# Optimization experiments

Measured on AMD Instinct MI355X. Metric: run time of the kernel, lower is better.

The kernel has to match this reference:

```python
import jax, jax.numpy as jnp
import numpy as np

HIDDEN = 1024
NUM_HEADS = 16
HEAD_DIM = HIDDEN // NUM_HEADS
ROPE_BASE = 10000.0


def _rope_cos_sin(seq_len, dtype):
    # inv_freq over even indices of head_dim
    inv_freq = 1.0 / (ROPE_BASE ** (jnp.arange(0, HEAD_DIM, 2, dtype=jnp.float32) / HEAD_DIM))
    t = jnp.arange(seq_len, dtype=jnp.float32)
    freqs = t[:, None] * inv_freq[None, :]            # (S, head_dim/2)
    emb = jnp.concatenate([freqs, freqs], axis=-1)    # (S, head_dim)
    cos = jnp.cos(emb)[None, None, :, :].astype(dtype)
    sin = jnp.sin(emb)[None, None, :, :].astype(dtype)
    return cos, sin


def _rotate_interleaved(x):
    # stack((-x[...,1::2], x[...,::2]), -1).flatten(-2) — interleaved pair rotation
    x1 = x[..., ::2]
    x2 = x[..., 1::2]
    return jnp.stack((-x2, x1), axis=-1).reshape(x.shape)


def _apply_rope(x, cos, sin):
    return x * cos + _rotate_interleaved(x) * sin


def setup_inputs() -> dict:
    key = jax.random.key(0)
    k0, k1, k2, k3, k4 = jax.random.split(key, 5)
    B, S = 2, 2048
    scale = 1.0 / np.sqrt(HIDDEN)
    return {
        "hidden_states": jax.random.normal(k0, (B, S, HIDDEN), dtype=jnp.float32),
        "Wq": jax.random.normal(k1, (HIDDEN, HIDDEN), dtype=jnp.float32) * scale,
        "Wk": jax.random.normal(k2, (HIDDEN, HIDDEN), dtype=jnp.float32) * scale,
        "Wv": jax.random.normal(k3, (HIDDEN, HIDDEN), dtype=jnp.float32) * scale,
        "Wo": jax.random.normal(k4, (HIDDEN, HIDDEN), dtype=jnp.float32) * scale,
    }


def reference(hidden_states, Wq, Wk, Wv, Wo):
    B, S, _ = hidden_states.shape
    # torch Linear: y = x @ W.T  (W is (out, in))
    def proj(x, W):
        y = jnp.einsum('bsd,ed->bse', x, W)
        return y.reshape(B, S, NUM_HEADS, HEAD_DIM).transpose(0, 2, 1, 3)  # (B,H,S,Dh)

    q = proj(hidden_states, Wq)
    k = proj(hidden_states, Wk)
    v = proj(hidden_states, Wv)

    cos, sin = _rope_cos_sin(S, hidden_states.dtype)
    q = _apply_rope(q, cos, sin)
    k = _apply_rope(k, cos, sin)

    scores = jnp.einsum('bhqd,bhkd->bhqk', q, k) / jnp.sqrt(jnp.asarray(HEAD_DIM, hidden_states.dtype))
    attn = jax.nn.softmax(scores, axis=-1)
    out = jnp.einsum('bhqk,bhkd->bhqd', attn, v)
    out = out.transpose(0, 2, 1, 3).reshape(B, S, HIDDEN)
    return jnp.einsum('bsd,ed->bse', out, Wo)
```

## Files before the change

kernel.cpp:

```cpp
#include <hip/hip_runtime.h>

typedef __attribute__((ext_vector_type(4)))  float  f32x4;
typedef __attribute__((ext_vector_type(16))) float  f32x16;
typedef __attribute__((ext_vector_type(8)))  short  s16x8;

__device__ __forceinline__ unsigned short f2bf(float f) {
    union { float f; unsigned u; } v; v.f = f;
    unsigned u = v.u + 0x7fffu + ((v.u >> 16) & 1u);
    return (unsigned short)(u >> 16);
}

__device__ __forceinline__ unsigned cvtpk(float lo, float hi_) {
    unsigned r;
    asm("v_cvt_pk_bf16_f32 %0, %1, %2" : "=v"(r) : "v"(lo), "v"(hi_));
    return r;
}

__device__ __forceinline__ void gl_lds16(const unsigned short* g, unsigned short* l) {
    __builtin_amdgcn_global_load_lds(
        (const __attribute__((address_space(1))) void*)g,
        (__attribute__((address_space(3))) void*)l, 16, 0, 0);
}

__device__ __forceinline__ f32x4 mfma16(s16x8 a, s16x8 b, f32x4 c) {
    return __builtin_amdgcn_mfma_f32_16x16x32_bf16(a, b, c, 0, 0, 0);
}
__device__ __forceinline__ f32x16 mfma32(s16x8 a, s16x8 b, f32x16 c) {
    return __builtin_amdgcn_mfma_f32_32x32x16_bf16(a, b, c, 0, 0, 0);
}

__global__ void k_convert(const float* __restrict__ s, unsigned short* __restrict__ d, int n4) {
    int i = blockIdx.x * 256 + threadIdx.x;
    if (i >= n4) return;
    float4 f = reinterpret_cast<const float4*>(s)[i];
    ushort4 o;
    o.x = f2bf(f.x); o.y = f2bf(f.y); o.z = f2bf(f.z); o.w = f2bf(f.w);
    reinterpret_cast<ushort4*>(d)[i] = o;
}

__global__ void k_rope_table(float* __restrict__ ct, float* __restrict__ st) {
    int i = blockIdx.x * 256 + threadIdx.x;
    int s = i >> 6, d = i & 63;
    float invf = powf(10000.0f, -(float)(d & 31) * (1.0f / 32.0f));
    float ang = (float)s * invf;
    float sv, cv;
    sincosf(ang, &sv, &cv);
    ct[i] = cv; st[i] = sv;
}

__global__ __launch_bounds__(256) void k_gemm_qkv(
    const unsigned short* __restrict__ Xb,
    const unsigned short* __restrict__ Wqb,
    const unsigned short* __restrict__ Wkb,
    const unsigned short* __restrict__ Wvb,
    const float* __restrict__ ct, const float* __restrict__ st,
    unsigned short* __restrict__ Qo, unsigned short* __restrict__ Ko,
    unsigned short* __restrict__ Vt)
{
    __shared__ __attribute__((aligned(16))) unsigned short As[128 * 32];
    __shared__ __attribute__((aligned(16))) unsigned short Bs[128 * 32];
    const int z = blockIdx.z;
    const int tid = threadIdx.x;
    const int lane = tid & 63;
    const int w  = tid >> 6;
    const int wm = (w >> 1) * 64, wn = (w & 1) * 64;
    const int r  = lane & 15, rg = lane >> 4;

    const unsigned short *Ap, *Bp;
    int m0, n0;
    if (z < 2) { Ap = Xb;  Bp = z ? Wkb : Wqb; m0 = blockIdx.x * 128; n0 = blockIdx.y * 128; }
    else       { Ap = Wvb; Bp = Xb;            m0 = blockIdx.y * 128; n0 = blockIdx.x * 128; }

    f32x4 acc[4][4];
    const f32x4 zf = {0.f, 0.f, 0.f, 0.f};
    #pragma unroll
    for (int i = 0; i < 4; i++)
        #pragma unroll
        for (int j = 0; j < 4; j++) acc[i][j] = zf;

    const unsigned short* ga = Ap + (size_t)(m0 + (tid >> 2)) * 1024 + (tid & 3) * 8;
    const unsigned short* gb = Bp + (size_t)(n0 + (tid >> 2)) * 1024 + (tid & 3) * 8;

    for (int k0 = 0; k0 < 1024; k0 += 32) {
        gl_lds16(ga + k0,             As + tid * 8);
        gl_lds16(ga + k0 + 64 * 1024, As + 2048 + tid * 8);
        gl_lds16(gb + k0,             Bs + tid * 8);
        gl_lds16(gb + k0 + 64 * 1024, Bs + 2048 + tid * 8);
        __syncthreads();
        s16x8 af[4], bfr[4];
        #pragma unroll
        for (int mi = 0; mi < 4; mi++) af[mi]  = *(const s16x8*)&As[(wm + mi * 16 + r) * 32 + rg * 8];
        #pragma unroll
        for (int ni = 0; ni < 4; ni++) bfr[ni] = *(const s16x8*)&Bs[(wn + ni * 16 + r) * 32 + rg * 8];
        #pragma unroll
        for (int mi = 0; mi < 4; mi++)
            #pragma unroll
            for (int ni = 0; ni < 4; ni++)
                acc[mi][ni] = mfma16(af[mi], bfr[ni], acc[mi][ni]);
        __syncthreads();
    }

    if (z < 2) {
        unsigned short* Out = z ? Ko : Qo;
        const float qscale = z ? 1.0f : 0.125f;
        #pragma unroll
        for (int mi = 0; mi < 4; mi++)
            #pragma unroll
            for (int ni = 0; ni < 4; ni++)
                #pragma unroll
                for (int rr = 0; rr < 4; rr++) {
                    float v = acc[mi][ni][rr];
                    float vp = __shfl_xor(v, 1);
                    int m = m0 + wm + mi * 16 + rg * 4 + rr;
                    int e = n0 + wn + ni * 16 + r;
                    int s = m & 2047, d = e & 63;
                    float c = ct[(s << 6) + d], sn = st[(s << 6) + d];
                    float sgn = (e & 1) ? 1.0f : -1.0f;
                    v = fmaf(v, c, sgn * vp * sn) * qscale;
                    int b = m >> 11, h = e >> 6;
                    Out[(((size_t)(b * 16 + h) * 2048 + s) << 6) + d] = f2bf(v);
                }
    } else {
        #pragma unroll
        for (int mi = 0; mi < 4; mi++)
            #pragma unroll
            for (int ni = 0; ni < 4; ni++)
                #pragma unroll
                for (int rr = 0; rr < 4; rr++) {
                    int e  = m0 + wm + mi * 16 + rg * 4 + rr;
                    int mm = n0 + wn + ni * 16 + r;
                    int b = mm >> 11, s = mm & 2047, h = e >> 6, d = e & 63;
                    Vt[((size_t)(b * 16 + h) * 64 + d) * 2048 + s] = f2bf(acc[mi][ni][rr]);
                }
    }
}

__global__ __launch_bounds__(512, 2) void k_attn(
    const unsigned short* __restrict__ Q,
    const unsigned short* __restrict__ K,
    const unsigned short* __restrict__ Vt,
    unsigned short* __restrict__ AO)
{
    __shared__ __attribute__((aligned(16))) unsigned short Ks[2][64 * 64];
    __shared__ __attribute__((aligned(16))) unsigned short Vs[2][64 * 64];
    const int bh = blockIdx.y;
    const int q0 = blockIdx.x * 256;
    const int tid = threadIdx.x, lane = tid & 63, w = tid >> 6;
    const int ln31 = lane & 31, hi = lane >> 5;
    const int swz = (ln31 & 7) << 3;
    const unsigned short* Qp = Q  + (size_t)bh * 2048 * 64;
    const unsigned short* Kp = K  + (size_t)bh * 2048 * 64;
    const unsigned short* Vp = Vt + (size_t)bh * 64 * 2048;

    s16x8 qf[4];
    #pragma unroll
    for (int ds = 0; ds < 4; ds++)
        qf[ds] = *(const s16x8*)&Qp[(size_t)(q0 + w * 32 + ln31) * 64 + ds * 16 + hi * 8];

    f32x16 o0, o1;
    #pragma unroll
    for (int r = 0; r < 16; r++) { o0[r] = 0.f; o1[r] = 0.f; }
    float mrun = -1e30f, lrun = 0.f;

    const int srow = tid >> 3;
    const int scol = ((tid & 7) * 8) ^ ((srow & 7) << 3);
    const unsigned short* gk = Kp + (size_t)srow * 64   + scol;
    const unsigned short* gv = Vp + (size_t)srow * 2048 + scol;
    const int t8 = tid * 8;

    gl_lds16(gk, &Ks[0][t8]);
    gl_lds16(gv, &Vs[0][t8]);
    asm volatile("s_waitcnt vmcnt(0)" ::: "memory");
    __syncthreads();

    int cur = 0;
    for (int t = 0; t < 32; ++t) {
        if (t < 31) {
            gl_lds16(gk + (size_t)(t + 1) * 4096, &Ks[cur ^ 1][t8]);
            gl_lds16(gv + (size_t)(t + 1) * 64,   &Vs[cur ^ 1][t8]);
        }
        const unsigned short* Kb = Ks[cur];
        const unsigned short* Vb = Vs[cur];

        f32x16 s0, s1;
        #pragma unroll
        for (int r = 0; r < 16; r++) { s0[r] = 0.f; s1[r] = 0.f; }
        __builtin_amdgcn_s_setprio(1);
        #pragma unroll
        for (int ds = 0; ds < 4; ds++) {
            s16x8 k0 = *(const s16x8*)&Kb[ ln31       * 64 + ((ds * 16 + hi * 8) ^ swz)];
            s16x8 k1 = *(const s16x8*)&Kb[(32 + ln31) * 64 + ((ds * 16 + hi * 8) ^ swz)];
            s0 = mfma32(k0, qf[ds], s0);
            s1 = mfma32(k1, qf[ds], s1);
        }
        __builtin_amdgcn_s_setprio(0);

        float tm = -1e30f;
        #pragma unroll
        for (int r = 0; r < 16; r++) tm = fmaxf(tm, fmaxf(s0[r], s1[r]));
        tm = fmaxf(tm, __shfl_xor(tm, 32));
        float mnew = fmaxf(mrun, tm);
        float al = __expf(mrun - mnew);
        mrun = mnew;
        float rs = 0.f;
        #pragma unroll
        for (int r = 0; r < 16; r++) { float p = __expf(s0[r] - mnew); s0[r] = p; rs += p; }
        #pragma unroll
        for (int r = 0; r < 16; r++) { float p = __expf(s1[r] - mnew); s1[r] = p; rs += p; }
        rs += __shfl_xor(rs, 32);
        lrun = lrun * al + rs;
        #pragma unroll
        for (int r = 0; r < 16; r++) { o0[r] *= al; o1[r] *= al; }

        s16x8 pa[4];
        #pragma unroll
        for (int ks = 0; ks < 4; ks++) {
            float x0, x1, x2, x3, x4, x5, x6, x7;
            if      (ks == 0) { x0=s0[0]; x1=s0[1]; x2=s0[2];  x3=s0[3];  x4=s0[4];  x5=s0[5];  x6=s0[6];  x7=s0[7];  }
            else if (ks == 1) { x0=s0[8]; x1=s0[9]; x2=s0[10]; x3=s0[11]; x4=s0[12]; x5=s0[13]; x6=s0[14]; x7=s0[15]; }
            else if (ks == 2) { x0=s1[0]; x1=s1[1]; x2=s1[2];  x3=s1[3];  x4=s1[4];  x5=s1[5];  x6=s1[6];  x7=s1[7];  }
            else              { x0=s1[8]; x1=s1[9]; x2=s1[10]; x3=s1[11]; x4=s1[12]; x5=s1[13]; x6=s1[14]; x7=s1[15]; }
            unsigned a  = cvtpk(x0, x1);
            unsigned a2 = cvtpk(x2, x3);
            unsigned b  = cvtpk(x4, x5);
            unsigned b2 = cvtpk(x6, x7);
            asm volatile("v_permlane32_swap_b32 %0, %1" : "+v"(a),  "+v"(b));
            asm volatile("v_permlane32_swap_b32 %0, %1" : "+v"(a2), "+v"(b2));
            union { s16x8 v; unsigned u[4]; } pu;
            pu.u[0] = a; pu.u[1] = a2; pu.u[2] = b; pu.u[3] = b2;
            pa[ks] = pu.v;
        }

        __builtin_amdgcn_s_setprio(1);
        #pragma unroll
        for (int ks = 0; ks < 4; ks++) {
            s16x8 v0 = *(const s16x8*)&Vb[ ln31       * 64 + ((ks * 16 + hi * 8) ^ swz)];
            s16x8 v1 = *(const s16x8*)&Vb[(32 + ln31) * 64 + ((ks * 16 + hi * 8) ^ swz)];
            o0 = mfma32(v0, pa[ks], o0);
            o1 = mfma32(v1, pa[ks], o1);
        }
        __builtin_amdgcn_s_setprio(0);

        __syncthreads();
        cur ^= 1;
    }

    float inv = 1.0f / lrun;
    const int b = bh >> 4, h = bh & 15;
    const int qg = q0 + w * 32 + ln31;
    size_t base = ((size_t)(b * 2048 + qg)) * 1024 + h * 64;
    #pragma unroll
    for (int dc = 0; dc < 2; dc++) {
        #pragma unroll
        for (int g = 0; g < 4; g++) {
            float y0, y1, y2, y3;
            if (dc == 0) { y0 = o0[4*g]; y1 = o0[4*g+1]; y2 = o0[4*g+2]; y3 = o0[4*g+3]; }
            else         { y0 = o1[4*g]; y1 = o1[4*g+1]; y2 = o1[4*g+2]; y3 = o1[4*g+3]; }
            unsigned lo  = cvtpk(y0 * inv, y1 * inv);
            unsigned hi2 = cvtpk(y2 * inv, y3 * inv);
            int d = dc * 32 + 8 * g + 4 * hi;
            uint2 stv; stv.x = lo; stv.y = hi2;
            *(uint2*)&AO[base + d] = stv;
        }
    }
}

__global__ __launch_bounds__(256) void k_gemm_out(
    const unsigned short* __restrict__ AOb,
    const unsigned short* __restrict__ Wob,
    float* __restrict__ Out)
{
    __shared__ __attribute__((aligned(16))) unsigned short As[128 * 32];
    __shared__ __attribute__((aligned(16))) unsigned short Bs[128 * 32];
    const int tid = threadIdx.x;
    const int lane = tid & 63;
    const int w  = tid >> 6;
    const int wm = (w >> 1) * 64, wn = (w & 1) * 64;
    const int r  = lane & 15, rg = lane >> 4;
    const int m0 = blockIdx.x * 128, n0 = blockIdx.y * 128;

    f32x4 acc[4][4];
    const f32x4 zf = {0.f, 0.f, 0.f, 0.f};
    #pragma unroll
    for (int i = 0; i < 4; i++)
        #pragma unroll
        for (int j = 0; j < 4; j++) acc[i][j] = zf;

    const unsigned short* ga = AOb + (size_t)(m0 + (tid >> 2)) * 1024 + (tid & 3) * 8;
    const unsigned short* gb = Wob + (size_t)(n0 + (tid >> 2)) * 1024 + (tid & 3) * 8;

    for (int k0 = 0; k0 < 1024; k0 += 32) {
        gl_lds16(ga + k0,             As + tid * 8);
        gl_lds16(ga + k0 + 64 * 1024, As + 2048 + tid * 8);
        gl_lds16(gb + k0,             Bs + tid * 8);
        gl_lds16(gb + k0 + 64 * 1024, Bs + 2048 + tid * 8);
        __syncthreads();
        s16x8 af[4], bfr[4];
        #pragma unroll
        for (int mi = 0; mi < 4; mi++) af[mi]  = *(const s16x8*)&As[(wm + mi * 16 + r) * 32 + rg * 8];
        #pragma unroll
        for (int ni = 0; ni < 4; ni++) bfr[ni] = *(const s16x8*)&Bs[(wn + ni * 16 + r) * 32 + rg * 8];
        #pragma unroll
        for (int mi = 0; mi < 4; mi++)
            #pragma unroll
            for (int ni = 0; ni < 4; ni++)
                acc[mi][ni] = mfma16(af[mi], bfr[ni], acc[mi][ni]);
        __syncthreads();
    }

    #pragma unroll
    for (int mi = 0; mi < 4; mi++)
        #pragma unroll
        for (int ni = 0; ni < 4; ni++)
            #pragma unroll
            for (int rr = 0; rr < 4; rr++) {
                int m = m0 + wm + mi * 16 + rg * 4 + rr;
                int e = n0 + wn + ni * 16 + r;
                Out[(size_t)m * 1024 + e] = acc[mi][ni][rr];
            }
}

extern "C" void kernel_launch(void* const* d_in, const int* in_sizes, int n_in,
                              void* d_out, int out_size, void* d_ws, size_t ws_size,
                              hipStream_t stream) {
    const float* X  = (const float*)d_in[0];
    const float* Wq = (const float*)d_in[1];
    const float* Wk = (const float*)d_in[2];
    const float* Wv = (const float*)d_in[3];
    const float* Wo = (const float*)d_in[4];
    float* Out = (float*)d_out;
    char* ws = (char*)d_ws;

    unsigned short* Xb   = (unsigned short*)(ws);
    unsigned short* Wqb  = (unsigned short*)(ws + 8388608);
    unsigned short* Wkb  = (unsigned short*)(ws + 10485760);
    unsigned short* Wvb  = (unsigned short*)(ws + 12582912);
    unsigned short* Wob  = (unsigned short*)(ws + 14680064);
    unsigned short* Qb   = (unsigned short*)(ws + 16777216);
    unsigned short* Kb   = (unsigned short*)(ws + 25165824);
    unsigned short* Vtb  = (unsigned short*)(ws + 33554432);
    unsigned short* AOb  = (unsigned short*)(ws + 41943040);
    float*          cosT = (float*)(ws + 50331648);
    float*          sinT = (float*)(ws + 50855936);

    k_convert<<<4096, 256, 0, stream>>>(X,  Xb,  1048576);
    k_convert<<<1024, 256, 0, stream>>>(Wq, Wqb, 262144);
    k_convert<<<1024, 256, 0, stream>>>(Wk, Wkb, 262144);
    k_convert<<<1024, 256, 0, stream>>>(Wv, Wvb, 262144);
    k_convert<<<1024, 256, 0, stream>>>(Wo, Wob, 262144);
    k_rope_table<<<512, 256, 0, stream>>>(cosT, sinT);
    k_gemm_qkv<<<dim3(32, 8, 3), 256, 0, stream>>>(Xb, Wqb, Wkb, Wvb, cosT, sinT, Qb, Kb, Vtb);
    k_attn<<<dim3(8, 32), 512, 0, stream>>>(Qb, Kb, Vtb, AOb);
    k_gemm_out<<<dim3(32, 8), 256, 0, stream>>>(AOb, Wob, Out);
}
```

Measured before the change: 226.4 us.

## Fuse prep kernels, use exp2 softmax with lazy rescale, shrink attention blocks

Merges the five conversion launches and the RoPE table launch into one prep kernel, cutting launch overhead. Folds log2(e) into the Q scale so softmax can use a native exp2, and skips rescaling the running output unless the max grows by more than a threshold. Reduces attention blocks to 256 threads covering 128 queries, giving 512 blocks and targeting three blocks per CU for better occupancy and balance. The lazy rescale keeps exponents bounded, at a small precision risk.

```diff
diff --git a/kernel.cpp b/kernel.cpp
--- a/kernel.cpp
+++ b/kernel.cpp
@@ -16,6 +16,14 @@
     return r;
 }
 
+__device__ __forceinline__ float ex2(float x) {
+#if __has_builtin(__builtin_amdgcn_exp2f)
+    return __builtin_amdgcn_exp2f(x);
+#else
+    return exp2f(x);
+#endif
+}
+
 __device__ __forceinline__ void gl_lds16(const unsigned short* g, unsigned short* l) {
     __builtin_amdgcn_global_load_lds(
         (const __attribute__((address_space(1))) void*)g,
@@ -29,23 +37,46 @@
     return __builtin_amdgcn_mfma_f32_32x32x16_bf16(a, b, c, 0, 0, 0);
 }
 
-__global__ void k_convert(const float* __restrict__ s, unsigned short* __restrict__ d, int n4) {
+__global__ __launch_bounds__(256) void k_prep(
+    const float* __restrict__ X,  const float* __restrict__ Wq,
+    const float* __restrict__ Wk, const float* __restrict__ Wv,
+    const float* __restrict__ Wo,
+    unsigned short* __restrict__ Xb,  unsigned short* __restrict__ Wqb,
+    unsigned short* __restrict__ Wkb, unsigned short* __restrict__ Wvb,
+    unsigned short* __restrict__ Wob,
+    float* __restrict__ ct, float* __restrict__ st)
+{
     int i = blockIdx.x * 256 + threadIdx.x;
-    if (i >= n4) return;
-    float4 f = reinterpret_cast<const float4*>(s)[i];
-    ushort4 o;
-    o.x = f2bf(f.x); o.y = f2bf(f.y); o.z = f2bf(f.z); o.w = f2bf(f.w);
-    reinterpret_cast<ushort4*>(d)[i] = o;
-}
-
-__global__ void k_rope_table(float* __restrict__ ct, float* __restrict__ st) {
-    int i = blockIdx.x * 256 + threadIdx.x;
-    int s = i >> 6, d = i & 63;
-    float invf = powf(10000.0f, -(float)(d & 31) * (1.0f / 32.0f));
-    float ang = (float)s * invf;
-    float sv, cv;
-    sincosf(ang, &sv, &cv);
-    ct[i] = cv; st[i] = sv;
+    if (i < 2097152) {
+        const float* s; unsigned short* d; int o;
+        if (i < 1048576) { s = X; d = Xb; o = i; }
+        else {
+            int j = i - 1048576;
+            int wsel = j >> 18; o = j & 262143;
+            s = (wsel == 0) ? Wq : (wsel == 1) ? Wk : (wsel == 2) ? Wv : Wo;
+            d = (wsel == 0) ? Wqb : (wsel == 1) ? Wkb : (wsel == 2) ? Wvb : Wob;
+        }
+        float4 f = reinterpret_cast<const float4*>(s)[o];
+        ushort4 u;
+        u.x = f2bf(f.x); u.y = f2bf(f.y); u.z = f2bf(f.z); u.w = f2bf(f.w);
+        reinterpret_cast<ushort4*>(d)[o] = u;
+    } else {
+        int j = i - 2097152;
+        int e0 = j << 2;
+        int sq = e0 >> 6, d0 = e0 & 63;
+        float4 cv, sv;
+        #pragma unroll
+        for (int k = 0; k < 4; k++) {
+            int d = d0 + k;
+            float invf = ex2(-(float)(d & 31) * 0.4152410118609203f);
+            float ang = (float)sq * invf;
+            float ss, cc;
+            sincosf(ang, &ss, &cc);
+            ((float*)&cv)[k] = cc; ((float*)&sv)[k] = ss;
+        }
+        *(float4*)&ct[e0] = cv;
+        *(float4*)&st[e0] = sv;
+    }
 }
 
 __global__ __launch_bounds__(256) void k_gemm_qkv(
@@ -102,7 +133,7 @@
 
     if (z < 2) {
         unsigned short* Out = z ? Ko : Qo;
-        const float qscale = z ? 1.0f : 0.125f;
+        const float qscale = z ? 1.0f : 0.18033688011112042f;
         #pragma unroll
         for (int mi = 0; mi < 4; mi++)
             #pragma unroll
@@ -135,7 +166,7 @@
     }
 }
 
-__global__ __launch_bounds__(512, 2) void k_attn(
+__global__ __launch_bounds__(256, 3) void k_attn(
     const unsigned short* __restrict__ Q,
     const unsigned short* __restrict__ K,
     const unsigned short* __restrict__ Vt,
@@ -144,7 +175,7 @@
     __shared__ __attribute__((aligned(16))) unsigned short Ks[2][64 * 64];
     __shared__ __attribute__((aligned(16))) unsigned short Vs[2][64 * 64];
     const int bh = blockIdx.y;
-    const int q0 = blockIdx.x * 256;
+    const int q0 = blockIdx.x * 128;
     const int tid = threadIdx.x, lane = tid & 63, w = tid >> 6;
     const int ln31 = lane & 31, hi = lane >> 5;
     const int swz = (ln31 & 7) << 3;
@@ -162,22 +193,31 @@
     for (int r = 0; r < 16; r++) { o0[r] = 0.f; o1[r] = 0.f; }
     float mrun = -1e30f, lrun = 0.f;
 
-    const int srow = tid >> 3;
-    const int scol = ((tid & 7) * 8) ^ ((srow & 7) << 3);
-    const unsigned short* gk = Kp + (size_t)srow * 64   + scol;
-    const unsigned short* gv = Vp + (size_t)srow * 2048 + scol;
-    const int t8 = tid * 8;
-
-    gl_lds16(gk, &Ks[0][t8]);
-    gl_lds16(gv, &Vs[0][t8]);
+    const int c1 = tid + 256;
+    const int sr0 = tid >> 3, sc0 = ((tid & 7) * 8) ^ ((sr0 & 7) << 3);
+    const int sr1 = c1 >> 3,  sc1 = ((c1 & 7) * 8) ^ ((sr1 & 7) << 3);
+    const unsigned short* gk0 = Kp + (size_t)sr0 * 64   + sc0;
+    const unsigned short* gk1 = Kp + (size_t)sr1 * 64   + sc1;
+    const unsigned short* gv0 = Vp + (size_t)sr0 * 2048 + sc0;
+    const unsigned short* gv1 = Vp + (size_t)sr1 * 2048 + sc1;
+    const int t80 = tid * 8, t81 = c1 * 8;
+
+    gl_lds16(gk0, &Ks[0][t80]);
+    gl_lds16(gk1, &Ks[0][t81]);
+    gl_lds16(gv0, &Vs[0][t80]);
+    gl_lds16(gv1, &Vs[0][t81]);
     asm volatile("s_waitcnt vmcnt(0)" ::: "memory");
     __syncthreads();
 
     int cur = 0;
     for (int t = 0; t < 32; ++t) {
         if (t < 31) {
-            gl_lds16(gk + (size_t)(t + 1) * 4096, &Ks[cur ^ 1][t8]);
-            gl_lds16(gv + (size_t)(t + 1) * 64,   &Vs[cur ^ 1][t8]);
+            size_t ok = (size_t)(t + 1) * 4096;
+            size_t ov = (size_t)(t + 1) * 64;
+            gl_lds16(gk0 + ok, &Ks[cur ^ 1][t80]);
+            gl_lds16(gk1 + ok, &Ks[cur ^ 1][t81]);
+            gl_lds16(gv0 + ov, &Vs[cur ^ 1][t80]);
+            gl_lds16(gv1 + ov, &Vs[cur ^ 1][t81]);
         }
         const unsigned short* Kb = Ks[cur];
         const unsigned short* Vb = Vs[cur];
@@ -199,18 +239,21 @@
         #pragma unroll
         for (int r = 0; r < 16; r++) tm = fmaxf(tm, fmaxf(s0[r], s1[r]));
         tm = fmaxf(tm, __shfl_xor(tm, 32));
-        float mnew = fmaxf(mrun, tm);
-        float al = __expf(mrun - mnew);
-        mrun = mnew;
+        if (!__all(tm <= mrun + 8.0f)) {
+            float mnew = fmaxf(mrun, tm);
+            float al = ex2(mrun - mnew);
+            mrun = mnew;
+            lrun *= al;
+            #pragma unroll
+            for (int r = 0; r < 16; r++) { o0[r] *= al; o1[r] *= al; }
+        }
         float rs = 0.f;
         #pragma unroll
-        for (int r = 0; r < 16; r++) { float p = __expf(s0[r] - mnew); s0[r] = p; rs += p; }
-        #pragma unroll
-        for (int r = 0; r < 16; r++) { float p = __expf(s1[r] - mnew); s1[r] = p; rs += p; }
+        for (int r = 0; r < 16; r++) { float p = ex2(s0[r] - mrun); s0[r] = p; rs += p; }
+        #pragma unroll
+        for (int r = 0; r < 16; r++) { float p = ex2(s1[r] - mrun); s1[r] = p; rs += p; }
         rs += __shfl_xor(rs, 32);
-        lrun = lrun * al + rs;
-        #pragma unroll
-        for (int r = 0; r < 16; r++) { o0[r] *= al; o1[r] *= al; }
+        lrun += rs;
 
         s16x8 pa[4];
         #pragma unroll
@@ -343,13 +386,8 @@
     float*          cosT = (float*)(ws + 50331648);
     float*          sinT = (float*)(ws + 50855936);
 
-    k_convert<<<4096, 256, 0, stream>>>(X,  Xb,  1048576);
-    k_convert<<<1024, 256, 0, stream>>>(Wq, Wqb, 262144);
-    k_convert<<<1024, 256, 0, stream>>>(Wk, Wkb, 262144);
-    k_convert<<<1024, 256, 0, stream>>>(Wv, Wvb, 262144);
-    k_convert<<<1024, 256, 0, stream>>>(Wo, Wob, 262144);
-    k_rope_table<<<512, 256, 0, stream>>>(cosT, sinT);
+    k_prep<<<8320, 256, 0, stream>>>(X, Wq, Wk, Wv, Wo, Xb, Wqb, Wkb, Wvb, Wob, cosT, sinT);
     k_gemm_qkv<<<dim3(32, 8, 3), 256, 0, stream>>>(Xb, Wqb, Wkb, Wvb, cosT, sinT, Qb, Kb, Vtb);
-    k_attn<<<dim3(8, 32), 512, 0, stream>>>(Qb, Kb, Vtb, AOb);
+    k_attn<<<dim3(16, 32), 256, 0, stream>>>(Qb, Kb, Vtb, AOb);
     k_gemm_out<<<dim3(32, 8), 256, 0, stream>>>(AOb, Wob, Out);
 }
```

New measurement: 213.0 us. -5.9%, faster.
